# Kernel tuning notes

Measured on AMD Instinct MI355X. Metric: run time of the kernel, lower is better.

Reference implementation:

```python
import jax, jax.numpy as jnp
import numpy as np

D_MODEL = 2048
N_HEADS = 32
N_KV = 8
D_K = D_MODEL // N_HEADS  # 64
N_REP = N_HEADS // N_KV   # 4


def setup_inputs() -> dict:
    key = jax.random.key(0)
    ks = jax.random.split(key, 5)
    B, T = 2, 2048
    s = 0.02
    return {
        "x": jax.random.normal(ks[0], (B, T, D_MODEL), dtype=jnp.float32),
        "Wq": jax.random.normal(ks[1], (D_MODEL, D_MODEL), dtype=jnp.float32) * s,
        "Wk": jax.random.normal(ks[2], (N_KV * D_K, D_MODEL), dtype=jnp.float32) * s,
        "Wv": jax.random.normal(ks[3], (N_KV * D_K, D_MODEL), dtype=jnp.float32) * s,
        "Wo": jax.random.normal(ks[4], (D_MODEL, D_MODEL), dtype=jnp.float32) * s,
    }


def reference(x, Wq, Wk, Wv, Wo):
    B, T, C = x.shape
    # projections (torch Linear: x @ W.T)
    Q = (x @ Wq.T).reshape(B, T, N_KV, N_REP, D_K)  # group query heads by kv group
    K = (x @ Wk.T).reshape(B, T, N_KV, D_K)
    V = (x @ Wv.T).reshape(B, T, N_KV, D_K)
    scale = 1.0 / jnp.sqrt(jnp.asarray(D_K, dtype=x.dtype))
    # scores: (B, n_kv, n_rep, T, T) == repeated-KV scores without materializing repeats
    scores = jnp.einsum('btgrd,bsgd->bgrts', Q, K) * scale
    causal_mask = jnp.triu(jnp.ones((T, T), dtype=bool), k=1)
    scores = jnp.where(causal_mask, -jnp.inf, scores)
    attn = jax.nn.softmax(scores, axis=-1)
    out = jnp.einsum('bgrts,bsgd->btgrd', attn, V).reshape(B, T, C)
    return out @ Wo.T
```

## Files before the change

kernel.cpp:

```cpp
#include <hip/hip_runtime.h>
#include <hip/hip_bf16.h>

typedef __attribute__((ext_vector_type(8))) short bf16x8;
typedef __attribute__((ext_vector_type(4))) float floatx4;

constexpr int D_MODEL = 2048;
constexpr int N_HEADS = 32;
constexpr int N_KV    = 8;
constexpr int B_      = 2;
constexpr int T_      = 2048;
constexpr int BT      = B_ * T_;
constexpr int NQKV    = 3072;

constexpr float Q_SCALE = 0.18033688011112042f;

__device__ __forceinline__ unsigned short f2bf(float f) {
    __hip_bfloat16 h = __float2bfloat16(f);
    return *reinterpret_cast<unsigned short*>(&h);
}

__device__ __forceinline__ void gll16(const void* g, void* l) {
    typedef const __attribute__((address_space(1))) unsigned int* gp_t;
    typedef __attribute__((address_space(3))) unsigned int* lp_t;
    __builtin_amdgcn_global_load_lds((gp_t)g, (lp_t)l, 16, 0, 0);
}

__global__ __launch_bounds__(256) void cvt_all(
        const float* __restrict__ x,  const float* __restrict__ wq,
        const float* __restrict__ wk, const float* __restrict__ wv,
        unsigned short* __restrict__ dst) {
    size_t i4 = (size_t)blockIdx.x * 256 + threadIdx.x;
    size_t e = i4 * 4;
    const float* src; size_t off;
    if (e < 8388608)        { src = x;  off = 0; }
    else if (e < 12582912)  { src = wq; off = 8388608; }
    else if (e < 13631488)  { src = wk; off = 12582912; }
    else                    { src = wv; off = 13631488; }
    float4 f = *reinterpret_cast<const float4*>(src + (e - off));
    unsigned short u[4] = {f2bf(f.x), f2bf(f.y), f2bf(f.z), f2bf(f.w)};
    reinterpret_cast<uint2*>(dst)[i4] = *reinterpret_cast<const uint2*>(u);
}

__global__ __launch_bounds__(256) void cvt_bf16(
        const float* __restrict__ src, unsigned short* __restrict__ dst, int n4) {
    int i = blockIdx.x * 256 + threadIdx.x;
    if (i < n4) {
        float4 f = reinterpret_cast<const float4*>(src)[i];
        unsigned short u[4] = {f2bf(f.x), f2bf(f.y), f2bf(f.z), f2bf(f.w)};
        reinterpret_cast<uint2*>(dst)[i] = *reinterpret_cast<const uint2*>(u);
    }
}

template<bool C_F32, bool SCALEQ>
__global__ __launch_bounds__(256) void gemm128(
        const unsigned short* __restrict__ A,
        const unsigned short* __restrict__ Bb,
        void* __restrict__ Cp,
        int M, int N, int K) {
    __shared__ unsigned short As[128 * 64];
    __shared__ unsigned short Bs[128 * 64];
    const int t = threadIdx.x;
    const int wave = t >> 6, lane = t & 63;
    const int l16 = lane & 15, quad = lane >> 4;
    const int wm = (wave & 1) * 64, wn = (wave >> 1) * 64;
    const int mtile = blockIdx.y * 128, ntile = blockIdx.x * 128;

    floatx4 acc[4][4] = {};

    for (int k0 = 0; k0 < K; k0 += 64) {
        __syncthreads();
#pragma unroll
        for (int c = 0; c < 4; c++) {
            int s = (c * 4 + wave) * 64 + lane;
            int row = s >> 3, k8 = (s & 7) ^ (row & 7);
            gll16(&A[(size_t)(mtile + row) * K + k0 + k8 * 8], &As[(c * 4 + wave) * 512]);
            gll16(&Bb[(size_t)(ntile + row) * K + k0 + k8 * 8], &Bs[(c * 4 + wave) * 512]);
        }
        __syncthreads();
#pragma unroll
        for (int kc = 0; kc < 2; kc++) {
            bf16x8 af[4], bfr[4];
#pragma unroll
            for (int i = 0; i < 4; i++) {
                int arow = wm + i * 16 + l16;
                af[i] = *reinterpret_cast<const bf16x8*>(
                    &As[(arow * 8 + ((kc * 4 + quad) ^ (arow & 7))) * 8]);
                int brow = wn + i * 16 + l16;
                bfr[i] = *reinterpret_cast<const bf16x8*>(
                    &Bs[(brow * 8 + ((kc * 4 + quad) ^ (brow & 7))) * 8]);
            }
#pragma unroll
            for (int i = 0; i < 4; i++)
#pragma unroll
                for (int jn = 0; jn < 4; jn++)
                    acc[i][jn] = __builtin_amdgcn_mfma_f32_16x16x32_bf16(
                        af[i], bfr[jn], acc[i][jn], 0, 0, 0);
        }
    }
    float cscale = (SCALEQ && ntile < 2048) ? Q_SCALE : 1.0f;
#pragma unroll
    for (int i = 0; i < 4; i++)
#pragma unroll
        for (int jn = 0; jn < 4; jn++)
#pragma unroll
            for (int r = 0; r < 4; r++) {
                int row = mtile + wm + i * 16 + quad * 4 + r;
                int col = ntile + wn + jn * 16 + l16;
                if constexpr (C_F32)
                    ((float*)Cp)[(size_t)row * N + col] = acc[i][jn][r];
                else
                    ((unsigned short*)Cp)[(size_t)row * N + col] =
                        f2bf(acc[i][jn][r] * cscale);
            }
}

__global__ __launch_bounds__(256) void vtrans(
        const unsigned short* __restrict__ QKV,
        unsigned short* __restrict__ Vt) {
    __shared__ unsigned short Ts[64][72];
    const int tb = blockIdx.x * 64;
    const int bg = blockIdx.y;
    const int b = bg >> 3, g = bg & 7;
    const int t = threadIdx.x;
#pragma unroll
    for (int it = 0; it < 2; it++) {
        int row = (t >> 3) + it * 32;
        int sl = t & 7;
        *reinterpret_cast<uint4*>(&Ts[row][sl * 8]) =
            *reinterpret_cast<const uint4*>(
                &QKV[(size_t)(b * T_ + tb + row) * NQKV + 2560 + g * 64 + sl * 8]);
    }
    __syncthreads();
#pragma unroll
    for (int it = 0; it < 2; it++) {
        int d = (t >> 3) + it * 32;
        int ks = t & 7;
        unsigned short u[8];
#pragma unroll
        for (int j = 0; j < 8; j++) u[j] = Ts[ks * 8 + j][d];
        *reinterpret_cast<uint4*>(&Vt[((size_t)bg * 64 + d) * T_ + tb + ks * 8]) =
            *reinterpret_cast<const uint4*>(u);
    }
}

__global__ __launch_bounds__(256) void attn4(
        const unsigned short* __restrict__ QKV,
        const unsigned short* __restrict__ Vt,
        unsigned short* __restrict__ O) {
    __shared__ unsigned short Ks[64 * 64];
    __shared__ unsigned short Vs[64 * 64];
    __shared__ unsigned short Ps[4][16 * 72];
    const int j  = blockIdx.x;
    const int bh = blockIdx.y;
    const int b = bh >> 5, h = bh & 31;
    const int g = h >> 2;
    const int t = threadIdx.x, wave = t >> 6, lane = t & 63;
    const int l16 = lane & 15, quad = lane >> 4;

    bf16x8 ones;
#pragma unroll
    for (int i = 0; i < 8; i++) ones[i] = (short)0x3F80;

    for (int pp = 0; pp < 2; pp++) {
        const int qtl = pp ? (31 - j) : j;
        const int qb0 = qtl * 64;
        const int qq = qb0 + wave * 16 + l16;
        const unsigned short* qptr = QKV + (size_t)(b * T_ + qq) * NQKV + h * 64;
        bf16x8 qf0 = *reinterpret_cast<const bf16x8*>(qptr + quad * 8);
        bf16x8 qf1 = *reinterpret_cast<const bf16x8*>(qptr + 32 + quad * 8);

        floatx4 o[4] = {};
        floatx4 lacc = {};

        for (int kt = 0; kt <= qtl; kt++) {
            const int kb = kt * 64;
            __syncthreads();
#pragma unroll
            for (int c = 0; c < 2; c++) {
                int s = (c * 4 + wave) * 64 + lane;
                int row = s >> 3, k8 = (s & 7) ^ (row & 7);
                gll16(&QKV[(size_t)(b * T_ + kb + row) * NQKV + 2048 + g * 64 + k8 * 8],
                      &Ks[(c * 4 + wave) * 512]);
                gll16(&Vt[((size_t)(b * 8 + g) * 64 + row) * T_ + kb + k8 * 8],
                      &Vs[(c * 4 + wave) * 512]);
            }
            __syncthreads();

            floatx4 sT[4];
#pragma unroll
            for (int nt = 0; nt < 4; nt++) {
                int krow = nt * 16 + l16;
                bf16x8 k0 = *reinterpret_cast<const bf16x8*>(
                    &Ks[(krow * 8 + (quad ^ (krow & 7))) * 8]);
                bf16x8 k1 = *reinterpret_cast<const bf16x8*>(
                    &Ks[(krow * 8 + ((4 + quad) ^ (krow & 7))) * 8]);
                floatx4 z = {};
                z = __builtin_amdgcn_mfma_f32_16x16x32_bf16(k0, qf0, z, 0, 0, 0);
                sT[nt] = __builtin_amdgcn_mfma_f32_16x16x32_bf16(k1, qf1, z, 0, 0, 0);
            }

            if (kt == qtl) {
#pragma unroll
                for (int nt = 0; nt < 4; nt++) {
                    unsigned short u[4];
#pragma unroll
                    for (int r = 0; r < 4; r++) {
                        float p = __builtin_amdgcn_exp2f(sT[nt][r]);
                        if ((kb + nt * 16 + quad * 4 + r) > qq) p = 0.f;
                        u[r] = f2bf(p);
                    }
                    *reinterpret_cast<uint2*>(&Ps[wave][l16 * 72 + nt * 16 + quad * 4]) =
                        *reinterpret_cast<const uint2*>(u);
                }
            } else {
#pragma unroll
                for (int nt = 0; nt < 4; nt++) {
                    unsigned short u[4];
#pragma unroll
                    for (int r = 0; r < 4; r++)
                        u[r] = f2bf(__builtin_amdgcn_exp2f(sT[nt][r]));
                    *reinterpret_cast<uint2*>(&Ps[wave][l16 * 72 + nt * 16 + quad * 4]) =
                        *reinterpret_cast<const uint2*>(u);
                }
            }

            bf16x8 p0 = *reinterpret_cast<const bf16x8*>(&Ps[wave][l16 * 72 + quad * 8]);
            bf16x8 p1 = *reinterpret_cast<const bf16x8*>(&Ps[wave][l16 * 72 + 32 + quad * 8]);
            lacc = __builtin_amdgcn_mfma_f32_16x16x32_bf16(p0, ones, lacc, 0, 0, 0);
            lacc = __builtin_amdgcn_mfma_f32_16x16x32_bf16(p1, ones, lacc, 0, 0, 0);
#pragma unroll
            for (int dt = 0; dt < 4; dt++) {
                int vrow = dt * 16 + l16;
                bf16x8 v0 = *reinterpret_cast<const bf16x8*>(
                    &Vs[(vrow * 8 + (quad ^ (vrow & 7))) * 8]);
                bf16x8 v1 = *reinterpret_cast<const bf16x8*>(
                    &Vs[(vrow * 8 + ((4 + quad) ^ (vrow & 7))) * 8]);
                o[dt] = __builtin_amdgcn_mfma_f32_16x16x32_bf16(p0, v0, o[dt], 0, 0, 0);
                o[dt] = __builtin_amdgcn_mfma_f32_16x16x32_bf16(p1, v1, o[dt], 0, 0, 0);
            }
        }

#pragma unroll
        for (int r = 0; r < 4; r++) {
            float inv = 1.0f / lacc[r];
            int row = b * T_ + qb0 + wave * 16 + quad * 4 + r;
#pragma unroll
            for (int dt = 0; dt < 4; dt++)
                O[(size_t)row * D_MODEL + h * 64 + dt * 16 + l16] = f2bf(o[dt][r] * inv);
        }
    }
}

extern "C" void kernel_launch(void* const* d_in, const int* in_sizes, int n_in,
                              void* d_out, int out_size, void* d_ws, size_t ws_size,
                              hipStream_t stream) {
    const float* x  = (const float*)d_in[0];
    const float* Wq = (const float*)d_in[1];
    const float* Wk = (const float*)d_in[2];
    const float* Wv = (const float*)d_in[3];
    const float* Wo = (const float*)d_in[4];

    unsigned short* xb   = (unsigned short*)d_ws;
    unsigned short* Wqkv = xb + (size_t)BT * D_MODEL;
    unsigned short* QKVo = Wqkv + (size_t)NQKV * D_MODEL;
    unsigned short* Vt   = QKVo + (size_t)BT * NQKV;
    unsigned short* Aw   = xb;
    unsigned short* Wob  = Wqkv;

    dim3 blk(256);
    cvt_all<<<dim3(14336), blk, 0, stream>>>(x, Wq, Wk, Wv, xb);
    gemm128<false, true><<<dim3(NQKV / 128, BT / 128), blk, 0, stream>>>(
        xb, Wqkv, QKVo, BT, NQKV, D_MODEL);
    cvt_bf16<<<dim3(D_MODEL * D_MODEL / 4 / 256), blk, 0, stream>>>(
        Wo, Wob, D_MODEL * D_MODEL / 4);
    vtrans<<<dim3(T_ / 64, B_ * N_KV), blk, 0, stream>>>(QKVo, Vt);
    attn4<<<dim3(16, B_ * N_HEADS), blk, 0, stream>>>(QKVo, Vt, Aw);
    gemm128<true, false><<<dim3(D_MODEL / 128, BT / 128), blk, 0, stream>>>(
        Aw, Wob, d_out, BT, D_MODEL, D_MODEL);
}
```

Measured before the change: 288.0 us.

## Double attention query tile to 128 rows per block, halving K/V loads

The attention kernel now gives each wave 32 query rows (two 16-row sub-tiles) so a block covers 128 queries. Each K/V tile loaded into LDS is therefore reused across twice as many queries, which halves global and LDS traffic per unit of work. The grid shrinks to 8 blocks per head (still paired for causal balance), and waves whose rows lie entirely above the causal diagonal skip compute. The cost is higher register and LDS use per block, fewer blocks in flight, and some idle waves on diagonal tiles.

Measured after the change: 281.8 us, median of 2. 2.1% less time.

```diff
diff --git a/kernel.cpp b/kernel.cpp
--- a/kernel.cpp
+++ b/kernel.cpp
@@ -143,13 +143,13 @@
     }
 }
 
-__global__ __launch_bounds__(256) void attn4(
+__global__ __launch_bounds__(256, 2) void attn5(
         const unsigned short* __restrict__ QKV,
         const unsigned short* __restrict__ Vt,
         unsigned short* __restrict__ O) {
     __shared__ unsigned short Ks[64 * 64];
     __shared__ unsigned short Vs[64 * 64];
-    __shared__ unsigned short Ps[4][16 * 72];
+    __shared__ unsigned short Ps[4][32 * 72];
     const int j  = blockIdx.x;
     const int bh = blockIdx.y;
     const int b = bh >> 5, h = bh & 31;
@@ -162,17 +162,24 @@
     for (int i = 0; i < 8; i++) ones[i] = (short)0x3F80;
 
     for (int pp = 0; pp < 2; pp++) {
-        const int qtl = pp ? (31 - j) : j;
-        const int qb0 = qtl * 64;
-        const int qq = qb0 + wave * 16 + l16;
-        const unsigned short* qptr = QKV + (size_t)(b * T_ + qq) * NQKV + h * 64;
-        bf16x8 qf0 = *reinterpret_cast<const bf16x8*>(qptr + quad * 8);
-        bf16x8 qf1 = *reinterpret_cast<const bf16x8*>(qptr + 32 + quad * 8);
-
-        floatx4 o[4] = {};
-        floatx4 lacc = {};
-
-        for (int kt = 0; kt <= qtl; kt++) {
+        const int qtl = pp ? (15 - j) : j;
+        const int q0  = qtl * 128;
+        const int qlo = q0 + wave * 32;
+
+        bf16x8 qf[2][2];
+#pragma unroll
+        for (int qb = 0; qb < 2; qb++) {
+            const unsigned short* qptr =
+                QKV + (size_t)(b * T_ + qlo + qb * 16 + l16) * NQKV + h * 64;
+            qf[qb][0] = *reinterpret_cast<const bf16x8*>(qptr + quad * 8);
+            qf[qb][1] = *reinterpret_cast<const bf16x8*>(qptr + 32 + quad * 8);
+        }
+
+        floatx4 o[2][4] = {};
+        floatx4 lacc[2] = {};
+
+        const int nkt = 2 * qtl + 2;
+        for (int kt = 0; kt < nkt; kt++) {
             const int kb = kt * 64;
             __syncthreads();
 #pragma unroll
@@ -186,48 +193,53 @@
             }
             __syncthreads();
 
-            floatx4 sT[4];
-#pragma unroll
-            for (int nt = 0; nt < 4; nt++) {
-                int krow = nt * 16 + l16;
+            if (kb > qlo + 31) continue;
+            const bool needmask = (kb + 63 > qlo);
+
+#pragma unroll
+            for (int km = 0; km < 4; km++) {
+                int krow = km * 16 + l16;
                 bf16x8 k0 = *reinterpret_cast<const bf16x8*>(
                     &Ks[(krow * 8 + (quad ^ (krow & 7))) * 8]);
                 bf16x8 k1 = *reinterpret_cast<const bf16x8*>(
                     &Ks[(krow * 8 + ((4 + quad) ^ (krow & 7))) * 8]);
-                floatx4 z = {};
-                z = __builtin_amdgcn_mfma_f32_16x16x32_bf16(k0, qf0, z, 0, 0, 0);
-                sT[nt] = __builtin_amdgcn_mfma_f32_16x16x32_bf16(k1, qf1, z, 0, 0, 0);
-            }
-
-            if (kt == qtl) {
-#pragma unroll
-                for (int nt = 0; nt < 4; nt++) {
+#pragma unroll
+                for (int qb = 0; qb < 2; qb++) {
+                    floatx4 z = {};
+                    z = __builtin_amdgcn_mfma_f32_16x16x32_bf16(k0, qf[qb][0], z, 0, 0, 0);
+                    z = __builtin_amdgcn_mfma_f32_16x16x32_bf16(k1, qf[qb][1], z, 0, 0, 0);
                     unsigned short u[4];
-#pragma unroll
-                    for (int r = 0; r < 4; r++) {
-                        float p = __builtin_amdgcn_exp2f(sT[nt][r]);
-                        if ((kb + nt * 16 + quad * 4 + r) > qq) p = 0.f;
-                        u[r] = f2bf(p);
+                    if (needmask) {
+                        int qq = qlo + qb * 16 + l16;
+#pragma unroll
+                        for (int r = 0; r < 4; r++) {
+                            float p = __builtin_amdgcn_exp2f(z[r]);
+                            if ((kb + km * 16 + quad * 4 + r) > qq) p = 0.f;
+                            u[r] = f2bf(p);
+                        }
+                    } else {
+#pragma unroll
+                        for (int r = 0; r < 4; r++)
+                            u[r] = f2bf(__builtin_amdgcn_exp2f(z[r]));
                     }
-                    *reinterpret_cast<uint2*>(&Ps[wave][l16 * 72 + nt * 16 + quad * 4]) =
+                    *reinterpret_cast<uint2*>(
+                        &Ps[wave][(qb * 16 + l16) * 72 + km * 16 + quad * 4]) =
                         *reinterpret_cast<const uint2*>(u);
                 }
-            } else {
-#pragma unroll
-                for (int nt = 0; nt < 4; nt++) {
-                    unsigned short u[4];
-#pragma unroll
-                    for (int r = 0; r < 4; r++)
-                        u[r] = f2bf(__builtin_amdgcn_exp2f(sT[nt][r]));
-                    *reinterpret_cast<uint2*>(&Ps[wave][l16 * 72 + nt * 16 + quad * 4]) =
-                        *reinterpret_cast<const uint2*>(u);
-                }
-            }
-
-            bf16x8 p0 = *reinterpret_cast<const bf16x8*>(&Ps[wave][l16 * 72 + quad * 8]);
-            bf16x8 p1 = *reinterpret_cast<const bf16x8*>(&Ps[wave][l16 * 72 + 32 + quad * 8]);
-            lacc = __builtin_amdgcn_mfma_f32_16x16x32_bf16(p0, ones, lacc, 0, 0, 0);
-            lacc = __builtin_amdgcn_mfma_f32_16x16x32_bf16(p1, ones, lacc, 0, 0, 0);
+            }
+
+            bf16x8 pf[2][2];
+#pragma unroll
+            for (int qb = 0; qb < 2; qb++) {
+#pragma unroll
+                for (int ks = 0; ks < 2; ks++)
+                    pf[qb][ks] = *reinterpret_cast<const bf16x8*>(
+                        &Ps[wave][(qb * 16 + l16) * 72 + ks * 32 + quad * 8]);
+                lacc[qb] = __builtin_amdgcn_mfma_f32_16x16x32_bf16(
+                    pf[qb][0], ones, lacc[qb], 0, 0, 0);
+                lacc[qb] = __builtin_amdgcn_mfma_f32_16x16x32_bf16(
+                    pf[qb][1], ones, lacc[qb], 0, 0, 0);
+            }
 #pragma unroll
             for (int dt = 0; dt < 4; dt++) {
                 int vrow = dt * 16 + l16;
@@ -235,19 +247,27 @@
                     &Vs[(vrow * 8 + (quad ^ (vrow & 7))) * 8]);
                 bf16x8 v1 = *reinterpret_cast<const bf16x8*>(
                     &Vs[(vrow * 8 + ((4 + quad) ^ (vrow & 7))) * 8]);
-                o[dt] = __builtin_amdgcn_mfma_f32_16x16x32_bf16(p0, v0, o[dt], 0, 0, 0);
-                o[dt] = __builtin_amdgcn_mfma_f32_16x16x32_bf16(p1, v1, o[dt], 0, 0, 0);
+#pragma unroll
+                for (int qb = 0; qb < 2; qb++) {
+                    o[qb][dt] = __builtin_amdgcn_mfma_f32_16x16x32_bf16(
+                        pf[qb][0], v0, o[qb][dt], 0, 0, 0);
+                    o[qb][dt] = __builtin_amdgcn_mfma_f32_16x16x32_bf16(
+                        pf[qb][1], v1, o[qb][dt], 0, 0, 0);
+                }
             }
         }
 
 #pragma unroll
-        for (int r = 0; r < 4; r++) {
-            float inv = 1.0f / lacc[r];
-            int row = b * T_ + qb0 + wave * 16 + quad * 4 + r;
-#pragma unroll
-            for (int dt = 0; dt < 4; dt++)
-                O[(size_t)row * D_MODEL + h * 64 + dt * 16 + l16] = f2bf(o[dt][r] * inv);
-        }
+        for (int qb = 0; qb < 2; qb++)
+#pragma unroll
+            for (int r = 0; r < 4; r++) {
+                float inv = 1.0f / lacc[qb][r];
+                int row = b * T_ + qlo + qb * 16 + quad * 4 + r;
+#pragma unroll
+                for (int dt = 0; dt < 4; dt++)
+                    O[(size_t)row * D_MODEL + h * 64 + dt * 16 + l16] =
+                        f2bf(o[qb][dt][r] * inv);
+            }
     }
 }
 
@@ -274,7 +294,7 @@
     cvt_bf16<<<dim3(D_MODEL * D_MODEL / 4 / 256), blk, 0, stream>>>(
         Wo, Wob, D_MODEL * D_MODEL / 4);
     vtrans<<<dim3(T_ / 64, B_ * N_KV), blk, 0, stream>>>(QKVo, Vt);
-    attn4<<<dim3(16, B_ * N_HEADS), blk, 0, stream>>>(QKVo, Vt, Aw);
+    attn5<<<dim3(8, B_ * N_HEADS), blk, 0, stream>>>(QKVo, Vt, Aw);
     gemm128<true, false><<<dim3(D_MODEL / 128, BT / 128), blk, 0, stream>>>(
         Aw, Wob, d_out, BT, D_MODEL, D_MODEL);
 }
```
